# Kernel optimization log

Hardware: AMD Instinct MI355X
Metric: run time of the kernel (lower is better)

## Reference

```python
import jax, jax.numpy as jnp
import numpy as np
from jax import lax

B, L, EMB, C, H, NTF = 512, 1024, 4, 64, 64, 200
D2 = 2 * H  # 128, bi-LSTM feature dim


def setup_inputs() -> dict:
    key = jax.random.key(0)
    ks = iter(jax.random.split(key, 48))
    r = lambda shape, s=0.05: jax.random.normal(next(ks), shape, jnp.float32) * s
    inp = {"DNA_x": jax.random.normal(next(ks), (B, L, EMB), jnp.float32)}
    # conv stack: channels 4 -> 64 -> 64, kernel 8
    inp["conv0_w"] = r((C, EMB, 8)); inp["conv0_b"] = r((C,))
    inp["bn0_g"] = 1.0 + r((C,)); inp["bn0_b"] = r((C,))
    inp["bn0_m"] = r((C,)); inp["bn0_v"] = jax.random.uniform(next(ks), (C,), jnp.float32, 0.5, 1.5)
    inp["conv1_w"] = r((C, C, 8)); inp["conv1_b"] = r((C,))
    inp["bn1_g"] = 1.0 + r((C,)); inp["bn1_b"] = r((C,))
    inp["bn1_m"] = r((C,)); inp["bn1_v"] = jax.random.uniform(next(ks), (C,), jnp.float32, 0.5, 1.5)
    # bidirectional LSTM, torch gate order (i, f, g, o)
    for d in ("f", "b"):
        inp[f"wih_{d}"] = r((4 * H, C)); inp[f"whh_{d}"] = r((4 * H, H))
        inp[f"bih_{d}"] = r((4 * H,)); inp[f"bhh_{d}"] = r((4 * H,))
    # Bahdanau attention: W1, W2: 128->128, V: 128->NTF
    inp["W1_w"] = r((D2, D2)); inp["W1_b"] = r((D2,))
    inp["W2_w"] = r((D2, D2)); inp["W2_b"] = r((D2,))
    inp["V_w"] = r((NTF, D2)); inp["V_b"] = r((NTF,))
    # per-TF heads stacked: Linear(128->64), Linear(64->1)
    inp["fc1_w"] = r((NTF, 64, D2)); inp["fc1_b"] = r((NTF, 64))
    inp["fc2_w"] = r((NTF, 64)); inp["fc2_b"] = r((NTF,))
    return inp


def _conv(x, w, b):  # x:[B,Cin,L], w:[Cout,Cin,K]
    y = lax.conv_general_dilated(x, w, (1,), "VALID",
                                 dimension_numbers=("NCH", "OIH", "NCH"))
    return y + b[:, None]


def _bn(x, g, b, m, v):  # eval-mode BatchNorm1d over channel dim
    return (x - m[:, None]) * (g[:, None] / jnp.sqrt(v[:, None] + 1e-5)) + b[:, None]


def _lstm(x, Wih, Whh, bih, bhh):  # x:[B,T,D] -> ([B,T,H], h_T:[B,H])
    Bn = x.shape[0]
    Hh = Whh.shape[1]
    bias = bih + bhh
    def step(carry, xt):
        h, c = carry
        g = xt @ Wih.T + h @ Whh.T + bias
        i, f, gg, o = jnp.split(g, 4, axis=-1)
        c = jax.nn.sigmoid(f) * c + jax.nn.sigmoid(i) * jnp.tanh(gg)
        h = jax.nn.sigmoid(o) * jnp.tanh(c)
        return (h, c), h
    init = (jnp.zeros((Bn, Hh), x.dtype), jnp.zeros((Bn, Hh), x.dtype))
    (hT, _), hs = lax.scan(step, init, jnp.swapaxes(x, 0, 1))
    return jnp.swapaxes(hs, 0, 1), hT


def reference(DNA_x, conv0_w, conv0_b, bn0_g, bn0_b, bn0_m, bn0_v,
              conv1_w, conv1_b, bn1_g, bn1_b, bn1_m, bn1_v,
              wih_f, whh_f, bih_f, bhh_f, wih_b, whh_b, bih_b, bhh_b,
              W1_w, W1_b, W2_w, W2_b, V_w, V_b,
              fc1_w, fc1_b, fc2_w, fc2_b):
    x = jnp.swapaxes(DNA_x, 1, 2)                      # [B,EMB,L]
    x = jax.nn.relu(_bn(_conv(x, conv0_w, conv0_b), bn0_g, bn0_b, bn0_m, bn0_v))
    x = lax.reduce_window(x, -jnp.inf, lax.max, (1, 1, 4), (1, 1, 4), "VALID")
    x = jax.nn.relu(_bn(_conv(x, conv1_w, conv1_b), bn1_g, bn1_b, bn1_m, bn1_v))
    x = jnp.swapaxes(x, 1, 2)                          # [B,T,C], T=247
    hf, hTf = _lstm(x, wih_f, whh_f, bih_f, bhh_f)
    hb, hTb = _lstm(x[:, ::-1, :], wih_b, whh_b, bih_b, bhh_b)
    values = jnp.concatenate([hf, hb[:, ::-1, :]], axis=-1)   # [B,T,2H]
    # torch h_n.view(B, 2H) on [2,B,H]: flat reshape (replicated exactly)
    h_n = jnp.stack([hTf, hTb], axis=0).reshape(values.shape[0], -1)
    # Bahdanau attention with NTF query heads
    score = jnp.tanh(values @ W1_w.T + W1_b + (h_n @ W2_w.T + W2_b)[:, None, :]) @ V_w.T + V_b
    aw = jax.nn.softmax(score, axis=1)                 # [B,T,NTF], softmax over time
    context = jnp.einsum("btd,btk->bkd", values, aw)   # [B,NTF,2H]
    # fused per-TF MLP heads: grouped GEMM over NTF
    h1 = jax.nn.relu(jnp.einsum("bkd,kod->bko", context, fc1_w) + fc1_b)
    out = jnp.einsum("bko,ko->bk", h1, fc2_w) + fc2_b  # [B,NTF]
    return out
```

## Files before the change

kernel.cpp:

```cpp
#include <hip/hip_runtime.h>
#include <math.h>

#define BB 512
#define LL 1024
#define EMB 4
#define CC 64
#define NTF 200
#define TT 247
#define LP 254
#define D2 128

typedef __attribute__((ext_vector_type(8))) short short8;
typedef __attribute__((ext_vector_type(4))) float f32x4;
typedef __attribute__((ext_vector_type(4))) unsigned int uint4v;

__device__ __forceinline__ float sigf(float x) {
  return __builtin_amdgcn_rcpf(1.0f + __expf(-x));
}
__device__ __forceinline__ float tanhff(float x) {
  return 1.0f - 2.0f * __builtin_amdgcn_rcpf(__expf(2.0f * x) + 1.0f);
}

__device__ __forceinline__ void lds_barrier() {
  __builtin_amdgcn_s_waitcnt(0xC07F);
  __builtin_amdgcn_s_barrier();
}

__device__ __forceinline__ unsigned short bfr(float f) {
  unsigned u = __builtin_bit_cast(unsigned, f);
  u += 0x7fffu + ((u >> 16) & 1u);
  return (unsigned short)(u >> 16);
}

__global__ __launch_bounds__(256) void k_cvt(const float* __restrict__ w0,
    const float* __restrict__ w1,
    const float* __restrict__ wihf, const float* __restrict__ whhf,
    const float* __restrict__ wihb, const float* __restrict__ whhb,
    const float* __restrict__ bihf, const float* __restrict__ bhhf,
    const float* __restrict__ bihb, const float* __restrict__ bhhb,
    const float* __restrict__ W1w, const float* __restrict__ Vw,
    const float* __restrict__ f1w,
    unsigned short* __restrict__ wbf0, unsigned short* __restrict__ wbf1r,
    unsigned short* __restrict__ wihbf, unsigned short* __restrict__ whhbf,
    float* __restrict__ lbias,
    unsigned short* __restrict__ W1bf, unsigned short* __restrict__ Vbf,
    unsigned short* __restrict__ f1bf)
{
  int i = blockIdx.x * 256 + threadIdx.x;
  if (i < 2048) wbf0[i] = bfr(w0[i]);
  if (i < 32768) {
    int co = i >> 9, k = (i >> 6) & 7, ci = i & 63;
    wbf1r[i] = bfr(w1[co * 512 + ci * 8 + k]);
  }
  if (i < 16384) {
    wihbf[i] = bfr(wihf[i]);
    wihbf[16384 + i] = bfr(wihb[i]);
    whhbf[i] = bfr(whhf[i]);
    whhbf[16384 + i] = bfr(whhb[i]);
    W1bf[i] = bfr(W1w[i]);
  }
  if (i < 26624) {
    int row = i >> 7;
    Vbf[i] = (row < NTF) ? bfr(Vw[i]) : (unsigned short)0;
  }
  if (i < 256) {
    lbias[i] = bihf[i] + bhhf[i];
    lbias[256 + i] = bihb[i] + bhhb[i];
  }
  if (i < 1638400) f1bf[i] = bfr(f1w[i]);
}

__global__ __launch_bounds__(256) void k_conv0m(const float* __restrict__ x,
    const unsigned short* __restrict__ wbf0,
    const float* __restrict__ b0, const float* __restrict__ g0,
    const float* __restrict__ be0, const float* __restrict__ m0,
    const float* __restrict__ v0, unsigned short* __restrict__ pbf)
{
  int b = blockIdx.x, l0 = blockIdx.y * 64;
  __shared__ float xs[71 * 4];
  __shared__ float sc[64], sb[64];
  int tid = threadIdx.x;
  for (int j = tid; j < 71; j += 256) {
    int l = l0 + j;
    float4 xv = (l < LL) ? *(const float4*)(x + ((size_t)b * LL + l) * EMB)
                         : make_float4(0.f, 0.f, 0.f, 0.f);
    *(float4*)(xs + j * 4) = xv;
  }
  if (tid < 64) {
    float s = g0[tid] * rsqrtf(v0[tid] + 1e-5f);
    sc[tid] = s;
    sb[tid] = (b0[tid] - m0[tid]) * s + be0[tid];
  }
  __syncthreads();
  int w = tid >> 6, lane = tid & 63, nl = lane & 15, quad = lane >> 4;
  const float* ap = xs + (w * 16 + nl) * 4 + quad;
  short8 af;
  #pragma unroll
  for (int j = 0; j < 8; ++j) af[j] = (short)bfr(ap[j * 4]);
  f32x4 acc[4];
  #pragma unroll
  for (int nt = 0; nt < 4; ++nt) {
    short8 bf = __builtin_bit_cast(short8,
        *(const uint4v*)(wbf0 + ((nt * 16 + nl) * 32 + quad * 8)));
    acc[nt] = (f32x4){0.f, 0.f, 0.f, 0.f};
    acc[nt] = __builtin_amdgcn_mfma_f32_16x16x32_bf16(af, bf, acc[nt], 0, 0, 0);
  }
  int t = (l0 >> 2) + w * 4 + quad;
  if (t < LP) {
    #pragma unroll
    for (int nt = 0; nt < 4; ++nt) {
      int c = nt * 16 + nl;
      float scc = sc[c], sbc = sb[c];
      float mx = -1e30f;
      #pragma unroll
      for (int r = 0; r < 4; ++r) mx = fmaxf(mx, acc[nt][r] * scc + sbc);
      pbf[((size_t)b * LP + t) * CC + c] = bfr(fmaxf(mx, 0.0f));
    }
  }
}

__global__ __launch_bounds__(256) void k_conv1m(const unsigned short* __restrict__ pbf,
    const unsigned short* __restrict__ wbf1r,
    const float* __restrict__ b1, const float* __restrict__ g1,
    const float* __restrict__ be1, const float* __restrict__ m1,
    const float* __restrict__ v1, unsigned short* __restrict__ x2bf)
{
  int b = blockIdx.x, t0 = blockIdx.y * 64;
  __shared__ __align__(16) unsigned short ps[71 * 72];
  __shared__ float sc[64], sb[64];
  int tid = threadIdx.x;
  for (int j = tid; j < 71 * 32; j += 256) {
    int tl = j >> 5, cu = j & 31;
    int t = t0 + tl;
    unsigned v = (t < LP) ? *(const unsigned*)(pbf + ((size_t)b * LP + t) * CC + cu * 2) : 0u;
    *(unsigned*)(&ps[tl * 72 + cu * 2]) = v;
  }
  if (tid < 64) {
    float s = g1[tid] * rsqrtf(v1[tid] + 1e-5f);
    sc[tid] = s;
    sb[tid] = (b1[tid] - m1[tid]) * s + be1[tid];
  }
  __syncthreads();
  int w = tid >> 6, lane = tid & 63, nl = lane & 15, quad = lane >> 4;
  int tlb = w * 16 + nl;
  f32x4 acc[4];
  #pragma unroll
  for (int nt = 0; nt < 4; ++nt) acc[nt] = (f32x4){0.f, 0.f, 0.f, 0.f};
  #pragma unroll
  for (int k8 = 0; k8 < 8; ++k8) {
    short8 af0 = __builtin_bit_cast(short8,
        *(const uint4v*)(&ps[(tlb + k8) * 72 + 0 + quad * 8]));
    short8 af1 = __builtin_bit_cast(short8,
        *(const uint4v*)(&ps[(tlb + k8) * 72 + 32 + quad * 8]));
    #pragma unroll
    for (int nt = 0; nt < 4; ++nt) {
      int co = nt * 16 + nl;
      short8 bf0 = __builtin_bit_cast(short8,
          *(const uint4v*)(wbf1r + (size_t)co * 512 + k8 * 64 + 0 + quad * 8));
      short8 bf1 = __builtin_bit_cast(short8,
          *(const uint4v*)(wbf1r + (size_t)co * 512 + k8 * 64 + 32 + quad * 8));
      acc[nt] = __builtin_amdgcn_mfma_f32_16x16x32_bf16(af0, bf0, acc[nt], 0, 0, 0);
      acc[nt] = __builtin_amdgcn_mfma_f32_16x16x32_bf16(af1, bf1, acc[nt], 0, 0, 0);
    }
  }
  #pragma unroll
  for (int nt = 0; nt < 4; ++nt) {
    int c = nt * 16 + nl;
    float scc = sc[c], sbc = sb[c];
    #pragma unroll
    for (int r = 0; r < 4; ++r) {
      int t = t0 + w * 16 + quad * 4 + r;
      if (t < TT)
        x2bf[((size_t)b * TT + t) * CC + c] = bfr(fmaxf(acc[nt][r] * scc + sbc, 0.0f));
    }
  }
}

__global__ __launch_bounds__(256) void k_lstm_m(const unsigned short* __restrict__ x2bf,
    const unsigned short* __restrict__ wihbf, const unsigned short* __restrict__ whhbf,
    const float* __restrict__ lbias,
    unsigned short* __restrict__ values, float* __restrict__ hT)
{
  int b0 = blockIdx.x * 16;
  int dir = blockIdx.y;
  int tid = threadIdx.x;
  int w = tid >> 6, lane = tid & 63, l15 = lane & 15, quad = lane >> 4;
  int h0 = w * 16;
  const unsigned short* wih = wihbf + dir * 16384;
  const unsigned short* whh = whhbf + dir * 16384;

  short8 bx[4][2], bh[4][2];
  float bias_v[4];
  #pragma unroll
  for (int g = 0; g < 4; ++g) {
    int row = g * 64 + h0 + l15;
    #pragma unroll
    for (int k = 0; k < 2; ++k) {
      bx[g][k] = __builtin_bit_cast(short8, *(const uint4v*)(wih + row * 64 + k * 32 + quad * 8));
      bh[g][k] = __builtin_bit_cast(short8, *(const uint4v*)(whh + row * 64 + k * 32 + quad * 8));
    }
    bias_v[g] = lbias[dir * 256 + g * 64 + h0 + l15];
  }

  __shared__ __align__(16) unsigned short xls[2][8][16 * 72];
  __shared__ __align__(16) unsigned short hist[8][16 * 72];
  for (int j = tid; j < 16 * 72; j += 256) hist[7][j] = 0;

  int bl = tid >> 4, d4 = tid & 15;
  const unsigned short* xrow = x2bf + ((size_t)(b0 + bl) * TT) * 64 + d4 * 4;

  uint2 xr[8];
  #pragma unroll
  for (int k = 0; k < 8; ++k) {
    int t = dir ? (TT - 1 - k) : k;
    xr[k] = *(const uint2*)(xrow + (size_t)t * 64);
  }
  #pragma unroll
  for (int k = 0; k < 8; ++k)
    *(uint2*)(&xls[0][k][bl * 72 + d4 * 4]) = xr[k];
  #pragma unroll
  for (int k = 0; k < 8; ++k) {
    int s = 8 + k;
    int t = dir ? (TT - 1 - s) : s;
    xr[k] = *(const uint2*)(xrow + (size_t)t * 64);
  }
  __syncthreads();

  float cst[4] = {0.f, 0.f, 0.f, 0.f};
  for (int c = 0; c < 31; ++c) {
    int buf = c & 1;
    #pragma unroll
    for (int sl = 0; sl < 8; ++sl) {
      int hp = (sl + 7) & 7;
      short8 ax0 = __builtin_bit_cast(short8, *(const uint4v*)(&xls[buf][sl][l15 * 72 + quad * 8]));
      short8 ax1 = __builtin_bit_cast(short8, *(const uint4v*)(&xls[buf][sl][l15 * 72 + 32 + quad * 8]));
      short8 ah0 = __builtin_bit_cast(short8, *(const uint4v*)(&hist[hp][l15 * 72 + quad * 8]));
      short8 ah1 = __builtin_bit_cast(short8, *(const uint4v*)(&hist[hp][l15 * 72 + 32 + quad * 8]));
      f32x4 aX[4], aH[4];
      #pragma unroll
      for (int g = 0; g < 4; ++g) {
        aX[g] = (f32x4){bias_v[g], bias_v[g], bias_v[g], bias_v[g]};
        aX[g] = __builtin_amdgcn_mfma_f32_16x16x32_bf16(ax0, bx[g][0], aX[g], 0, 0, 0);
        aX[g] = __builtin_amdgcn_mfma_f32_16x16x32_bf16(ax1, bx[g][1], aX[g], 0, 0, 0);
        aH[g] = (f32x4){0.f, 0.f, 0.f, 0.f};
        aH[g] = __builtin_amdgcn_mfma_f32_16x16x32_bf16(ah0, bh[g][0], aH[g], 0, 0, 0);
        aH[g] = __builtin_amdgcn_mfma_f32_16x16x32_bf16(ah1, bh[g][1], aH[g], 0, 0, 0);
      }
      #pragma unroll
      for (int r = 0; r < 4; ++r) {
        float ig = sigf(aX[0][r] + aH[0][r]);
        float fg = sigf(aX[1][r] + aH[1][r]);
        float gg = tanhff(aX[2][r] + aH[2][r]);
        float og = sigf(aX[3][r] + aH[3][r]);
        cst[r] = fg * cst[r] + ig * gg;
        float hh = og * tanhff(cst[r]);
        hist[sl][(quad * 4 + r) * 72 + h0 + l15] = bfr(hh);
        if (c == 30 && sl == 6) {
          int bglob = b0 + quad * 4 + r;
          hT[((size_t)dir * BB + bglob) * 64 + h0 + l15] = hh;
        }
      }
      lds_barrier();
    }
    uint4v dv[4];
    #pragma unroll
    for (int i = 0; i < 4; ++i) {
      int flat = i * 256 + tid;
      int sl = flat >> 7, wb = (flat >> 3) & 15, c8 = flat & 7;
      dv[i] = *(const uint4v*)(&hist[sl][wb * 72 + c8 * 8]);
    }
    #pragma unroll
    for (int i = 0; i < 4; ++i) {
      int flat = i * 256 + tid;
      int sl = flat >> 7, wb = (flat >> 3) & 15, c8 = flat & 7;
      int s = c * 8 + sl;
      if (s < TT) {
        int t = dir ? (TT - 1 - s) : s;
        *(uint4v*)(values + ((size_t)(b0 + wb) * TT + t) * D2 + dir * 64 + c8 * 8) = dv[i];
      }
    }
    if (c < 30) {
      #pragma unroll
      for (int k = 0; k < 8; ++k)
        *(uint2*)(&xls[1 - buf][k][bl * 72 + d4 * 4]) = xr[k];
      #pragma unroll
      for (int k = 0; k < 8; ++k) {
        int s2 = (c + 2) * 8 + k;
        if (s2 > TT - 1) s2 = TT - 1;
        int t2 = dir ? (TT - 1 - s2) : s2;
        xr[k] = *(const uint2*)(xrow + (size_t)t2 * 64);
      }
    }
    lds_barrier();
  }
}

__global__ __launch_bounds__(128) void k_q2(const float* __restrict__ hT,
    const float* __restrict__ W2, const float* __restrict__ W2b,
    float* __restrict__ q2)
{
  int b = blockIdx.x;
  int tid = threadIdx.x;
  __shared__ float4 hn4[32];
  ((float*)hn4)[tid] = hT[(size_t)b * 128 + tid];
  __syncthreads();
  const float4* w4 = (const float4*)(W2 + (size_t)tid * 128);
  float a = W2b[tid];
  #pragma unroll
  for (int j = 0; j < 32; ++j) {
    float4 w = w4[j]; float4 h = hn4[j];
    a += w.x * h.x + w.y * h.y + w.z * h.z + w.w * h.w;
  }
  q2[(size_t)b * 128 + tid] = a;
}

__global__ __launch_bounds__(256) void k_score_m(const unsigned short* __restrict__ vbf,
    const unsigned short* __restrict__ W1bf, const float* __restrict__ W1b,
    const float* __restrict__ q2, const unsigned short* __restrict__ Vbf,
    const float* __restrict__ Vb, unsigned short* __restrict__ scoreT)
{
  int b = blockIdx.x, t0 = blockIdx.y * 64;
  int tid = threadIdx.x, w = tid >> 6, lane = tid & 63, l15 = lane & 15, quad = lane >> 4;
  __shared__ unsigned short us[64 * 136];
  __shared__ unsigned short sc2[64 * 213];
  const unsigned short* arow = vbf + ((size_t)b * TT + t0 + w * 16 + l15) * 128;
  short8 ax[4];
  #pragma unroll
  for (int ks = 0; ks < 4; ++ks)
    ax[ks] = __builtin_bit_cast(short8, *(const uint4v*)(arow + ks * 32 + quad * 8));
  #pragma unroll
  for (int nt = 0; nt < 8; ++nt) {
    int n = nt * 16 + l15;
    float base = W1b[n] + q2[(size_t)b * 128 + n];
    f32x4 acc = (f32x4){base, base, base, base};
    #pragma unroll
    for (int ks = 0; ks < 4; ++ks) {
      short8 bf = __builtin_bit_cast(short8,
          *(const uint4v*)(W1bf + (size_t)n * 128 + ks * 32 + quad * 8));
      acc = __builtin_amdgcn_mfma_f32_16x16x32_bf16(ax[ks], bf, acc, 0, 0, 0);
    }
    #pragma unroll
    for (int r = 0; r < 4; ++r)
      us[(w * 16 + quad * 4 + r) * 136 + nt * 16 + l15] = bfr(tanhff(acc[r]));
  }
  __syncthreads();
  short8 au[4];
  #pragma unroll
  for (int ks = 0; ks < 4; ++ks)
    au[ks] = __builtin_bit_cast(short8, *(const uint4v*)(&us[(w * 16 + l15) * 136 + ks * 32 + quad * 8]));
  for (int nt2 = 0; nt2 < 13; ++nt2) {
    int n = nt2 * 16 + l15;
    float b2 = (n < NTF) ? Vb[n] : 0.0f;
    f32x4 a2 = (f32x4){b2, b2, b2, b2};
    #pragma unroll
    for (int ks = 0; ks < 4; ++ks) {
      short8 bf = __builtin_bit_cast(short8,
          *(const uint4v*)(Vbf + (size_t)n * 128 + ks * 32 + quad * 8));
      a2 = __builtin_amdgcn_mfma_f32_16x16x32_bf16(au[ks], bf, a2, 0, 0, 0);
    }
    #pragma unroll
    for (int r = 0; r < 4; ++r) {
      int tl = w * 16 + quad * 4 + r;
      sc2[tl * 213 + n] = bfr(a2[r]);
    }
  }
  __syncthreads();
  int tg = tid & 3;
  #pragma unroll
  for (int pp = 0; pp < 4; ++pp) {
    int nrow = pp * 64 + (tid >> 2);
    if (nrow < NTF) {
      unsigned uu[8];
      #pragma unroll
      for (int k2 = 0; k2 < 8; ++k2) {
        unsigned lo = sc2[(tg * 16 + k2 * 2) * 213 + nrow];
        unsigned hi = sc2[(tg * 16 + k2 * 2 + 1) * 213 + nrow];
        uu[k2] = lo | (hi << 16);
      }
      size_t dst = ((size_t)b * 208 + nrow) * 256 + t0 + tg * 16;
      *(uint4v*)(scoreT + dst) = (uint4v){uu[0], uu[1], uu[2], uu[3]};
      *(uint4v*)(scoreT + dst + 8) = (uint4v){uu[4], uu[5], uu[6], uu[7]};
    }
  }
}

__global__ __launch_bounds__(256) void k_softmax(unsigned short* __restrict__ scoreT,
    float* __restrict__ sinv)
{
  int b = blockIdx.x, nc = blockIdx.y;
  int tid = threadIdx.x;
  int n = nc * 64 + (tid >> 2), tg = tid & 3;
  if (n >= NTF) return;
  unsigned short* row = scoreT + ((size_t)b * 208 + n) * 256 + tg * 64;
  uint4v ld[8];
  #pragma unroll
  for (int i = 0; i < 8; ++i) ld[i] = *(const uint4v*)(row + i * 8);
  float m = -1e30f;
  #pragma unroll
  for (int i = 0; i < 8; ++i) {
    #pragma unroll
    for (int u = 0; u < 4; ++u) {
      unsigned xv = ld[i][u];
      int t0 = tg * 64 + i * 8 + u * 2;
      float a = __builtin_bit_cast(float, xv << 16);
      float c = __builtin_bit_cast(float, xv & 0xffff0000u);
      if (t0 < TT) m = fmaxf(m, a);
      if (t0 + 1 < TT) m = fmaxf(m, c);
    }
  }
  m = fmaxf(m, __shfl_xor(m, 1, 64));
  m = fmaxf(m, __shfl_xor(m, 2, 64));
  float s = 0.0f;
  #pragma unroll
  for (int i = 0; i < 8; ++i) {
    uint4v ov;
    #pragma unroll
    for (int u = 0; u < 4; ++u) {
      unsigned xv = ld[i][u];
      int t0 = tg * 64 + i * 8 + u * 2;
      float a = __builtin_bit_cast(float, xv << 16);
      float c = __builtin_bit_cast(float, xv & 0xffff0000u);
      float ea = (t0 < TT) ? __expf(a - m) : 0.0f;
      float ec = (t0 + 1 < TT) ? __expf(c - m) : 0.0f;
      s += ea + ec;
      ov[u] = (unsigned)bfr(ea) | ((unsigned)bfr(ec) << 16);
    }
    *(uint4v*)(row + i * 8) = ov;
  }
  s += __shfl_xor(s, 1, 64);
  s += __shfl_xor(s, 2, 64);
  if (tg == 0) sinv[(size_t)b * NTF + n] = __builtin_amdgcn_rcpf(s);
}

__global__ __launch_bounds__(256) void k_ctx_m(const unsigned short* __restrict__ vbf,
    const unsigned short* __restrict__ scoreT, const float* __restrict__ sinv,
    unsigned short* __restrict__ ctxbf)
{
  int b = blockIdx.x;
  int tid = threadIdx.x, w = tid >> 6, lane = tid & 63, l15 = lane & 15, quad = lane >> 4;
  __shared__ __align__(16) unsigned short vt[128 * 264];
  __shared__ float sls[208];
  for (int flat = tid; flat < 247 * 64; flat += 256) {
    int t = flat >> 6, dp = flat & 63;
    unsigned v = *(const unsigned*)(vbf + ((size_t)b * TT + t) * D2 + dp * 2);
    vt[(dp * 2) * 264 + t] = (unsigned short)(v & 0xffffu);
    vt[(dp * 2 + 1) * 264 + t] = (unsigned short)(v >> 16);
  }
  for (int j = tid; j < 128 * 9; j += 256) {
    int d = j / 9, t = 247 + (j % 9);
    vt[d * 264 + t] = 0;
  }
  for (int j = tid; j < 208; j += 256) sls[j] = (j < NTF) ? sinv[(size_t)b * NTF + j] : 0.0f;
  __syncthreads();

  const unsigned short* abase = scoreT + (size_t)b * 208 * 256;
  for (int mi = 0; mi < 4; ++mi) {
    int mt = w + 4 * mi;
    if (mt >= 13) continue;
    const unsigned short* arow = abase + (size_t)(mt * 16 + l15) * 256;
    short8 af[8];
    #pragma unroll
    for (int ks = 0; ks < 8; ++ks)
      af[ks] = __builtin_bit_cast(short8, *(const uint4v*)(arow + ks * 32 + quad * 8));
    f32x4 acc[8];
    #pragma unroll
    for (int dt = 0; dt < 8; ++dt) {
      acc[dt] = (f32x4){0.f, 0.f, 0.f, 0.f};
      #pragma unroll
      for (int ks = 0; ks < 8; ++ks) {
        short8 bf = __builtin_bit_cast(short8,
            *(const uint4v*)(&vt[(dt * 16 + l15) * 264 + ks * 32 + quad * 8]));
        acc[dt] = __builtin_amdgcn_mfma_f32_16x16x32_bf16(af[ks], bf, acc[dt], 0, 0, 0);
      }
    }
    #pragma unroll
    for (int r = 0; r < 4; ++r) {
      int n = mt * 16 + quad * 4 + r;
      if (n < NTF) {
        float rs = sls[n];
        #pragma unroll
        for (int dt = 0; dt < 8; ++dt)
          ctxbf[((size_t)b * NTF + n) * D2 + dt * 16 + l15] = bfr(acc[dt][r] * rs);
      }
    }
  }
}

__global__ __launch_bounds__(256) void k_heads_m(const unsigned short* __restrict__ ctxbf,
    const unsigned short* __restrict__ f1bf, const float* __restrict__ fc1b,
    const float* __restrict__ fc2w, const float* __restrict__ fc2b,
    float* __restrict__ out)
{
  int n = blockIdx.x;
  int b0 = blockIdx.y * 128;
  int tid = threadIdx.x, w = tid >> 6, lane = tid & 63, l15 = lane & 15, quad = lane >> 4;
  short8 bfr_[4][4];
  float f1bv[4], f2v[4];
  #pragma unroll
  for (int nt = 0; nt < 4; ++nt) {
    int o = nt * 16 + l15;
    #pragma unroll
    for (int ks = 0; ks < 4; ++ks)
      bfr_[nt][ks] = __builtin_bit_cast(short8,
          *(const uint4v*)(f1bf + ((size_t)n * 64 + o) * 128 + ks * 32 + quad * 8));
    f1bv[nt] = fc1b[n * 64 + o];
    f2v[nt] = fc2w[n * 64 + o];
  }
  float f2b = fc2b[n];
  #pragma unroll
  for (int mi = 0; mi < 2; ++mi) {
    int m16 = (w * 2 + mi) * 16;
    const unsigned short* arow = ctxbf + ((size_t)(b0 + m16 + l15) * NTF + n) * 128;
    short8 af[4];
    #pragma unroll
    for (int ks = 0; ks < 4; ++ks)
      af[ks] = __builtin_bit_cast(short8, *(const uint4v*)(arow + ks * 32 + quad * 8));
    f32x4 acc[4];
    #pragma unroll
    for (int nt = 0; nt < 4; ++nt) {
      acc[nt] = (f32x4){0.f, 0.f, 0.f, 0.f};
      #pragma unroll
      for (int ks = 0; ks < 4; ++ks)
        acc[nt] = __builtin_amdgcn_mfma_f32_16x16x32_bf16(af[ks], bfr_[nt][ks], acc[nt], 0, 0, 0);
    }
    #pragma unroll
    for (int r = 0; r < 4; ++r) {
      float part = 0.0f;
      #pragma unroll
      for (int nt = 0; nt < 4; ++nt)
        part += fmaxf(acc[nt][r] + f1bv[nt], 0.0f) * f2v[nt];
      part += __shfl_xor(part, 1, 64);
      part += __shfl_xor(part, 2, 64);
      part += __shfl_xor(part, 4, 64);
      part += __shfl_xor(part, 8, 64);
      if (l15 == 0) {
        int bb = b0 + m16 + quad * 4 + r;
        out[(size_t)bb * NTF + n] = part + f2b;
      }
    }
  }
}

extern "C" void kernel_launch(void* const* d_in, const int* in_sizes, int n_in,
                              void* d_out, int out_size, void* d_ws, size_t ws_size,
                              hipStream_t stream)
{
  const float* x    = (const float*)d_in[0];
  const float* c0w  = (const float*)d_in[1];
  const float* c0b  = (const float*)d_in[2];
  const float* g0   = (const float*)d_in[3];
  const float* be0  = (const float*)d_in[4];
  const float* m0   = (const float*)d_in[5];
  const float* v0   = (const float*)d_in[6];
  const float* c1w  = (const float*)d_in[7];
  const float* c1b  = (const float*)d_in[8];
  const float* g1   = (const float*)d_in[9];
  const float* be1  = (const float*)d_in[10];
  const float* m1   = (const float*)d_in[11];
  const float* v1   = (const float*)d_in[12];
  const float* wihf = (const float*)d_in[13];
  const float* whhf = (const float*)d_in[14];
  const float* bihf = (const float*)d_in[15];
  const float* bhhf = (const float*)d_in[16];
  const float* wihb = (const float*)d_in[17];
  const float* whhb = (const float*)d_in[18];
  const float* bihb = (const float*)d_in[19];
  const float* bhhb = (const float*)d_in[20];
  const float* W1w  = (const float*)d_in[21];
  const float* W1b  = (const float*)d_in[22];
  const float* W2w  = (const float*)d_in[23];
  const float* W2b  = (const float*)d_in[24];
  const float* Vw   = (const float*)d_in[25];
  const float* Vb   = (const float*)d_in[26];
  const float* f1w  = (const float*)d_in[27];
  const float* f1b  = (const float*)d_in[28];
  const float* f2w  = (const float*)d_in[29];
  const float* f2b  = (const float*)d_in[30];

  float* ws = (float*)d_ws;
  unsigned short* scoreT = (unsigned short*)ws;
  unsigned short* pbf  = (unsigned short*)ws;
  unsigned short* x2bf = (unsigned short*)(ws + 8323072);
  unsigned short* vbf  = (unsigned short*)(ws + 25292800);
  float* hT     = ws + 33387520;
  float* q2     = ws + 33453056;
  float* sinv   = ws + 33518592;
  unsigned short* ctxbf = (unsigned short*)(ws + 33620992);
  unsigned short* wbf0  = (unsigned short*)(ws + 46728192);
  unsigned short* wbf1r = (unsigned short*)(ws + 46729216);
  unsigned short* wihbf = (unsigned short*)(ws + 46745600);
  unsigned short* whhbf = (unsigned short*)(ws + 46761984);
  float* lbias          = ws + 46778368;
  unsigned short* W1bf  = (unsigned short*)(ws + 46778880);
  unsigned short* Vbf   = (unsigned short*)(ws + 46787072);
  unsigned short* f1bf  = (unsigned short*)(ws + 46800384);
  float* out    = (float*)d_out;

  k_cvt<<<dim3(6400), 256, 0, stream>>>(c0w, c1w, wihf, whhf, wihb, whhb,
                                        bihf, bhhf, bihb, bhhb, W1w, Vw, f1w,
                                        wbf0, wbf1r, wihbf, whhbf, lbias, W1bf, Vbf, f1bf);
  k_conv0m<<<dim3(BB, 16), 256, 0, stream>>>(x, wbf0, c0b, g0, be0, m0, v0, pbf);
  k_conv1m<<<dim3(BB, 4), 256, 0, stream>>>(pbf, wbf1r, c1b, g1, be1, m1, v1, x2bf);
  k_lstm_m<<<dim3(BB / 16, 2), 256, 0, stream>>>(x2bf, wihbf, whhbf, lbias, vbf, hT);
  k_q2<<<dim3(BB), 128, 0, stream>>>(hT, W2w, W2b, q2);
  k_score_m<<<dim3(BB, 4), 256, 0, stream>>>(vbf, W1bf, W1b, q2, Vbf, Vb, scoreT);
  k_softmax<<<dim3(BB, 4), 256, 0, stream>>>(scoreT, sinv);
  k_ctx_m<<<dim3(BB), 256, 0, stream>>>(vbf, scoreT, sinv, ctxbf);
  k_heads_m<<<dim3(NTF, 4), 256, 0, stream>>>(ctxbf, f1bf, f1b, f2w, f2b, out);
}
```

Before: 523.3 us.

## Fuse softmax into context kernel, prescale LSTM gates for exp2, transpose ctx layout

The standalone softmax kernel is removed. The context kernel now computes the row max and sum from the bf16 scores, then recomputes the exponentials while building the MFMA A-fragments, which saves a write and reread of the score matrix and one launch. The LSTM weights and biases are prescaled by log2(e), or 2·log2(e) for the g gate, so the cell can use raw exp2 and merge the input and g gate reciprocals into one. The context output is stored n-major so the heads kernel reads it contiguously, and the weight-conversion kernel converts f1 with float4 loads over fewer blocks. The cost is that the exponentials are computed twice in the context kernel, and rounding changes slightly.

```diff
diff --git a/kernel.cpp b/kernel.cpp
--- a/kernel.cpp
+++ b/kernel.cpp
@@ -14,11 +14,18 @@
 typedef __attribute__((ext_vector_type(4))) float f32x4;
 typedef __attribute__((ext_vector_type(4))) unsigned int uint4v;
 
-__device__ __forceinline__ float sigf(float x) {
-  return __builtin_amdgcn_rcpf(1.0f + __expf(-x));
-}
+#define L2E  1.4426950408889634f
+#define TL2E 2.8853900817779268f
+
 __device__ __forceinline__ float tanhff(float x) {
   return 1.0f - 2.0f * __builtin_amdgcn_rcpf(__expf(2.0f * x) + 1.0f);
+}
+
+__device__ __forceinline__ float ex2(float x) {
+  return __builtin_amdgcn_exp2f(x);
+}
+__device__ __forceinline__ float tanh2(float y) {
+  return 1.0f - 2.0f * __builtin_amdgcn_rcpf(ex2(y) + 1.0f);
 }
 
 __device__ __forceinline__ void lds_barrier() {
@@ -53,10 +60,11 @@
     wbf1r[i] = bfr(w1[co * 512 + ci * 8 + k]);
   }
   if (i < 16384) {
-    wihbf[i] = bfr(wihf[i]);
-    wihbf[16384 + i] = bfr(wihb[i]);
-    whhbf[i] = bfr(whhf[i]);
-    whhbf[16384 + i] = bfr(whhb[i]);
+    float s = ((i >> 12) == 2) ? TL2E : L2E;
+    wihbf[i] = bfr(wihf[i] * s);
+    wihbf[16384 + i] = bfr(wihb[i] * s);
+    whhbf[i] = bfr(whhf[i] * s);
+    whhbf[16384 + i] = bfr(whhb[i] * s);
     W1bf[i] = bfr(W1w[i]);
   }
   if (i < 26624) {
@@ -64,10 +72,20 @@
     Vbf[i] = (row < NTF) ? bfr(Vw[i]) : (unsigned short)0;
   }
   if (i < 256) {
-    lbias[i] = bihf[i] + bhhf[i];
-    lbias[256 + i] = bihb[i] + bhhb[i];
-  }
-  if (i < 1638400) f1bf[i] = bfr(f1w[i]);
+    float s = ((i >> 6) == 2) ? TL2E : L2E;
+    lbias[i] = (bihf[i] + bhhf[i]) * s;
+    lbias[256 + i] = (bihb[i] + bhhb[i]) * s;
+  }
+  {
+    int i4 = i * 4;
+    if (i4 < 1638400) {
+      float4 v = *(const float4*)(f1w + i4);
+      f1bf[i4 + 0] = bfr(v.x);
+      f1bf[i4 + 1] = bfr(v.y);
+      f1bf[i4 + 2] = bfr(v.z);
+      f1bf[i4 + 3] = bfr(v.w);
+    }
+  }
 }
 
 __global__ __launch_bounds__(256) void k_conv0m(const float* __restrict__ x,
@@ -248,12 +266,18 @@
       }
       #pragma unroll
       for (int r = 0; r < 4; ++r) {
-        float ig = sigf(aX[0][r] + aH[0][r]);
-        float fg = sigf(aX[1][r] + aH[1][r]);
-        float gg = tanhff(aX[2][r] + aH[2][r]);
-        float og = sigf(aX[3][r] + aH[3][r]);
-        cst[r] = fg * cst[r] + ig * gg;
-        float hh = og * tanhff(cst[r]);
+        float yi = aX[0][r] + aH[0][r];
+        float yf = aX[1][r] + aH[1][r];
+        float yg = aX[2][r] + aH[2][r];
+        float yo = aX[3][r] + aH[3][r];
+        float Fi = ex2(-yi);
+        float Ff = ex2(-yf);
+        float Eg = ex2(yg);
+        float fg = __builtin_amdgcn_rcpf(1.0f + Ff);
+        float igg = (Eg - 1.0f) * __builtin_amdgcn_rcpf((1.0f + Fi) * (Eg + 1.0f));
+        cst[r] = fg * cst[r] + igg;
+        float og = __builtin_amdgcn_rcpf(1.0f + ex2(-yo));
+        float hh = og * tanh2(cst[r] * TL2E);
         hist[sl][(quad * 4 + r) * 72 + h0 + l15] = bfr(hh);
         if (c == 30 && sl == 6) {
           int bglob = b0 + quad * 4 + r;
@@ -384,62 +408,14 @@
   }
 }
 
-__global__ __launch_bounds__(256) void k_softmax(unsigned short* __restrict__ scoreT,
-    float* __restrict__ sinv)
-{
-  int b = blockIdx.x, nc = blockIdx.y;
-  int tid = threadIdx.x;
-  int n = nc * 64 + (tid >> 2), tg = tid & 3;
-  if (n >= NTF) return;
-  unsigned short* row = scoreT + ((size_t)b * 208 + n) * 256 + tg * 64;
-  uint4v ld[8];
-  #pragma unroll
-  for (int i = 0; i < 8; ++i) ld[i] = *(const uint4v*)(row + i * 8);
-  float m = -1e30f;
-  #pragma unroll
-  for (int i = 0; i < 8; ++i) {
-    #pragma unroll
-    for (int u = 0; u < 4; ++u) {
-      unsigned xv = ld[i][u];
-      int t0 = tg * 64 + i * 8 + u * 2;
-      float a = __builtin_bit_cast(float, xv << 16);
-      float c = __builtin_bit_cast(float, xv & 0xffff0000u);
-      if (t0 < TT) m = fmaxf(m, a);
-      if (t0 + 1 < TT) m = fmaxf(m, c);
-    }
-  }
-  m = fmaxf(m, __shfl_xor(m, 1, 64));
-  m = fmaxf(m, __shfl_xor(m, 2, 64));
-  float s = 0.0f;
-  #pragma unroll
-  for (int i = 0; i < 8; ++i) {
-    uint4v ov;
-    #pragma unroll
-    for (int u = 0; u < 4; ++u) {
-      unsigned xv = ld[i][u];
-      int t0 = tg * 64 + i * 8 + u * 2;
-      float a = __builtin_bit_cast(float, xv << 16);
-      float c = __builtin_bit_cast(float, xv & 0xffff0000u);
-      float ea = (t0 < TT) ? __expf(a - m) : 0.0f;
-      float ec = (t0 + 1 < TT) ? __expf(c - m) : 0.0f;
-      s += ea + ec;
-      ov[u] = (unsigned)bfr(ea) | ((unsigned)bfr(ec) << 16);
-    }
-    *(uint4v*)(row + i * 8) = ov;
-  }
-  s += __shfl_xor(s, 1, 64);
-  s += __shfl_xor(s, 2, 64);
-  if (tg == 0) sinv[(size_t)b * NTF + n] = __builtin_amdgcn_rcpf(s);
-}
-
 __global__ __launch_bounds__(256) void k_ctx_m(const unsigned short* __restrict__ vbf,
-    const unsigned short* __restrict__ scoreT, const float* __restrict__ sinv,
+    const unsigned short* __restrict__ scoreT,
     unsigned short* __restrict__ ctxbf)
 {
   int b = blockIdx.x;
   int tid = threadIdx.x, w = tid >> 6, lane = tid & 63, l15 = lane & 15, quad = lane >> 4;
   __shared__ __align__(16) unsigned short vt[128 * 264];
-  __shared__ float sls[208];
+  __shared__ float sm[208], sls[208];
   for (int flat = tid; flat < 247 * 64; flat += 256) {
     int t = flat >> 6, dp = flat & 63;
     unsigned v = *(const unsigned*)(vbf + ((size_t)b * TT + t) * D2 + dp * 2);
@@ -450,7 +426,50 @@
     int d = j / 9, t = 247 + (j % 9);
     vt[d * 264 + t] = 0;
   }
-  for (int j = tid; j < 208; j += 256) sls[j] = (j < NTF) ? sinv[(size_t)b * NTF + j] : 0.0f;
+  {
+    int nn = tid >> 2, tg = tid & 3;
+    #pragma unroll
+    for (int pp = 0; pp < 4; ++pp) {
+      int n = pp * 64 + nn;
+      if (n < 208) {
+        const unsigned short* row = scoreT + ((size_t)b * 208 + n) * 256 + tg * 64;
+        uint4v ld[8];
+        #pragma unroll
+        for (int i = 0; i < 8; ++i) ld[i] = *(const uint4v*)(row + i * 8);
+        float m = -1e30f;
+        #pragma unroll
+        for (int i = 0; i < 8; ++i) {
+          #pragma unroll
+          for (int u = 0; u < 4; ++u) {
+            unsigned xv = ld[i][u];
+            int t0 = tg * 64 + i * 8 + u * 2;
+            float a = __builtin_bit_cast(float, xv << 16);
+            float cc = __builtin_bit_cast(float, xv & 0xffff0000u);
+            if (t0 < TT) m = fmaxf(m, a);
+            if (t0 + 1 < TT) m = fmaxf(m, cc);
+          }
+        }
+        m = fmaxf(m, __shfl_xor(m, 1, 64));
+        m = fmaxf(m, __shfl_xor(m, 2, 64));
+        float s = 0.0f;
+        #pragma unroll
+        for (int i = 0; i < 8; ++i) {
+          #pragma unroll
+          for (int u = 0; u < 4; ++u) {
+            unsigned xv = ld[i][u];
+            int t0 = tg * 64 + i * 8 + u * 2;
+            float a = __builtin_bit_cast(float, xv << 16);
+            float cc = __builtin_bit_cast(float, xv & 0xffff0000u);
+            if (t0 < TT) s += ex2((a - m) * L2E);
+            if (t0 + 1 < TT) s += ex2((cc - m) * L2E);
+          }
+        }
+        s += __shfl_xor(s, 1, 64);
+        s += __shfl_xor(s, 2, 64);
+        if (tg == 0) { sm[n] = m; sls[n] = __builtin_amdgcn_rcpf(s); }
+      }
+    }
+  }
   __syncthreads();
 
   const unsigned short* abase = scoreT + (size_t)b * 208 * 256;
@@ -458,10 +477,24 @@
     int mt = w + 4 * mi;
     if (mt >= 13) continue;
     const unsigned short* arow = abase + (size_t)(mt * 16 + l15) * 256;
+    float mrow = sm[mt * 16 + l15];
     short8 af[8];
     #pragma unroll
-    for (int ks = 0; ks < 8; ++ks)
-      af[ks] = __builtin_bit_cast(short8, *(const uint4v*)(arow + ks * 32 + quad * 8));
+    for (int ks = 0; ks < 8; ++ks) {
+      uint4v raw = *(const uint4v*)(arow + ks * 32 + quad * 8);
+      uint4v pk;
+      #pragma unroll
+      for (int u = 0; u < 4; ++u) {
+        unsigned xv = raw[u];
+        int t0 = ks * 32 + quad * 8 + u * 2;
+        float a = __builtin_bit_cast(float, xv << 16);
+        float cc = __builtin_bit_cast(float, xv & 0xffff0000u);
+        float pa = (t0 < TT) ? ex2((a - mrow) * L2E) : 0.0f;
+        float pc = (t0 + 1 < TT) ? ex2((cc - mrow) * L2E) : 0.0f;
+        pk[u] = (unsigned)bfr(pa) | ((unsigned)bfr(pc) << 16);
+      }
+      af[ks] = __builtin_bit_cast(short8, pk);
+    }
     f32x4 acc[8];
     #pragma unroll
     for (int dt = 0; dt < 8; ++dt) {
@@ -480,7 +513,7 @@
         float rs = sls[n];
         #pragma unroll
         for (int dt = 0; dt < 8; ++dt)
-          ctxbf[((size_t)b * NTF + n) * D2 + dt * 16 + l15] = bfr(acc[dt][r] * rs);
+          ctxbf[((size_t)n * BB + b) * D2 + dt * 16 + l15] = bfr(acc[dt][r] * rs);
       }
     }
   }
@@ -510,7 +543,7 @@
   #pragma unroll
   for (int mi = 0; mi < 2; ++mi) {
     int m16 = (w * 2 + mi) * 16;
-    const unsigned short* arow = ctxbf + ((size_t)(b0 + m16 + l15) * NTF + n) * 128;
+    const unsigned short* arow = ctxbf + ((size_t)n * BB + (b0 + m16 + l15)) * 128;
     short8 af[4];
     #pragma unroll
     for (int ks = 0; ks < 4; ++ks)
@@ -584,7 +617,6 @@
   unsigned short* vbf  = (unsigned short*)(ws + 25292800);
   float* hT     = ws + 33387520;
   float* q2     = ws + 33453056;
-  float* sinv   = ws + 33518592;
   unsigned short* ctxbf = (unsigned short*)(ws + 33620992);
   unsigned short* wbf0  = (unsigned short*)(ws + 46728192);
   unsigned short* wbf1r = (unsigned short*)(ws + 46729216);
@@ -596,7 +628,7 @@
   unsigned short* f1bf  = (unsigned short*)(ws + 46800384);
   float* out    = (float*)d_out;
 
-  k_cvt<<<dim3(6400), 256, 0, stream>>>(c0w, c1w, wihf, whhf, wihb, whhb,
+  k_cvt<<<dim3(1600), 256, 0, stream>>>(c0w, c1w, wihf, whhf, wihb, whhb,
                                         bihf, bhhf, bihb, bhhb, W1w, Vw, f1w,
                                         wbf0, wbf1r, wihbf, whhbf, lbias, W1bf, Vbf, f1bf);
   k_conv0m<<<dim3(BB, 16), 256, 0, stream>>>(x, wbf0, c0b, g0, be0, m0, v0, pbf);
@@ -604,7 +636,6 @@
   k_lstm_m<<<dim3(BB / 16, 2), 256, 0, stream>>>(x2bf, wihbf, whhbf, lbias, vbf, hT);
   k_q2<<<dim3(BB), 128, 0, stream>>>(hT, W2w, W2b, q2);
   k_score_m<<<dim3(BB, 4), 256, 0, stream>>>(vbf, W1bf, W1b, q2, Vbf, Vb, scoreT);
-  k_softmax<<<dim3(BB, 4), 256, 0, stream>>>(scoreT, sinv);
-  k_ctx_m<<<dim3(BB), 256, 0, stream>>>(vbf, scoreT, sinv, ctxbf);
+  k_ctx_m<<<dim3(BB), 256, 0, stream>>>(vbf, scoreT, ctxbf);
   k_heads_m<<<dim3(NTF, 4), 256, 0, stream>>>(ctxbf, f1bf, f1b, f2w, f2b, out);
 }
```

After: 481.4 us. 1.09x faster.
